# Kernel optimization log

Hardware: AMD Instinct MI355X
Metric: run time of the kernel (lower is better)

The kernel has to match this reference:

```python
import jax, jax.numpy as jnp
import numpy as np

K = 5  # kernel_size
PAD = K // 2


def _median_filter(x):
    # x: [B,1,H,W]; reflect pad then 5x5 window median (lower median of 25 elems == true median)
    B, C, H, W = x.shape
    xp = jnp.pad(x, ((0, 0), (0, 0), (PAD, PAD), (PAD, PAD)), mode='reflect')
    windows = jnp.stack([xp[:, :, dy:dy + H, dx:dx + W]
                         for dy in range(K) for dx in range(K)], axis=0)
    return jnp.median(windows, axis=0)


def _gaussian_kernel(sigma):
    c = K // 2
    coords = jnp.arange(K, dtype=jnp.float32) - c
    d2 = coords[:, None] ** 2 + coords[None, :] ** 2  # [K,K]
    kern = jnp.exp(-d2 / (2.0 * sigma ** 2)) / (2.0 * jnp.pi * sigma ** 2)
    kern = kern / kern.sum()
    return kern[None, None]  # [1,1,K,K] (OIHW, single channel, groups=1)


def setup_inputs() -> dict:
    key = jax.random.key(0)
    img = jax.random.normal(key, (8, 1024, 1024), dtype=jnp.float32)
    sigma = jnp.float32(4.0)  # learnable parameter of the Gaussian filter
    return {"img": img, "sigma": sigma}


def reference(img, sigma):
    x = img[:, None]           # [B,1,H,W]
    x = _median_filter(x)      # [B,1,H,W]
    kern = _gaussian_kernel(sigma)
    x = jax.lax.conv_general_dilated(
        x, kern, window_strides=(1, 1),
        padding=[(PAD, PAD), (PAD, PAD)],
        dimension_numbers=('NCHW', 'OIHW', 'NCHW'))
    return x[:, 0]             # [B,H,W]
```

## Files before the change

### kernel.cpp

```cpp
#include <hip/hip_runtime.h>

#define HH 1024
#define WW 1024
#define NIMG 8
#define TROWS 16

__device__ __forceinline__ float med3f(float a, float b, float c) {
    return __builtin_amdgcn_fmed3f(a, b, c);
}
__device__ __forceinline__ float min3f(float a, float b, float c) {
    return fminf(fminf(a, b), c);
}
__device__ __forceinline__ float max3f(float a, float b, float c) {
    return fmaxf(fmaxf(a, b), c);
}

__device__ __forceinline__ void top2(float a, float b, float c, float d, float e,
                                     float& r3, float& r4) {
    float m3 = med3f(a, b, c);
    float h3 = max3f(a, b, c);
    float s2 = med3f(m3, h3, d);
    float s3 = fmaxf(h3, d);
    r3 = med3f(s2, s3, e);
    r4 = fmaxf(s3, e);
}
__device__ __forceinline__ void bot2(float a, float b, float c, float d, float e,
                                     float& r0, float& r1) {
    float l3 = min3f(a, b, c);
    float m3 = med3f(a, b, c);
    float s0 = fminf(l3, d);
    float s1 = med3f(l3, m3, d);
    r0 = fminf(s0, e);
    r1 = med3f(s0, s1, e);
}
__device__ __forceinline__ void top3(float a, float b, float c, float d, float e,
                                     float& r2, float& r3, float& r4) {
    float l3 = min3f(a, b, c);
    float m3 = med3f(a, b, c);
    float h3 = max3f(a, b, c);
    float s1 = med3f(l3, m3, d);
    float s2 = med3f(m3, h3, d);
    float s3 = fmaxf(h3, d);
    r2 = med3f(s1, s2, e);
    r3 = med3f(s2, s3, e);
    r4 = fmaxf(s3, e);
}
__device__ __forceinline__ void bot3(float a, float b, float c, float d, float e,
                                     float& r0, float& r1, float& r2) {
    float l3 = min3f(a, b, c);
    float m3 = med3f(a, b, c);
    float h3 = max3f(a, b, c);
    float s0 = fminf(l3, d);
    float s1 = med3f(l3, m3, d);
    float s2 = med3f(m3, h3, d);
    r0 = fminf(s0, e);
    r1 = med3f(s0, s1, e);
    r2 = med3f(s1, s2, e);
}
__device__ __forceinline__ void mid3(float a, float b, float c, float d, float e,
                                     float& r1, float& r2, float& r3) {
    float l3 = min3f(a, b, c);
    float m3 = med3f(a, b, c);
    float h3 = max3f(a, b, c);
    float s0 = fminf(l3, d);
    float s1 = med3f(l3, m3, d);
    float s2 = med3f(m3, h3, d);
    float s3 = fmaxf(h3, d);
    r1 = med3f(s0, s1, e);
    r2 = med3f(s1, s2, e);
    r3 = med3f(s2, s3, e);
}

__device__ __forceinline__ void loadrow(const float* __restrict__ base, int r,
                                        int tid, int x0, float (&d)[8]) {
    const int rr = (r < 0) ? -r : (r >= HH ? 2 * HH - 2 - r : r);
    const float* rp = base + (size_t)rr * WW;
    const float4 A = *reinterpret_cast<const float4*>(rp + (tid == 0   ? x0 : x0 - 4));
    const float4 B = *reinterpret_cast<const float4*>(rp + x0);
    const float4 C = *reinterpret_cast<const float4*>(rp + (tid == 255 ? x0 : x0 + 4));
    d[0] = (tid == 0)   ? B.z : A.z;
    d[1] = (tid == 0)   ? B.y : A.w;
    d[2] = B.x; d[3] = B.y; d[4] = B.z; d[5] = B.w;
    d[6] = (tid == 255) ? B.z : C.x;
    d[7] = (tid == 255) ? B.y : C.y;
}

__device__ __forceinline__ void med4net(const float (&S0)[8], const float (&S1)[8],
                                        const float (&S2)[8], const float (&S3)[8],
                                        const float (&S4)[8], float (&med)[4]) {
    #pragma unroll
    for (int j = 0; j < 4; ++j) {
        float r03, r04, r12, r13, r14, r21, r22, r23, r30, r31, r32, r40, r41;
        top2(S0[j], S0[j+1], S0[j+2], S0[j+3], S0[j+4], r03, r04);
        top3(S1[j], S1[j+1], S1[j+2], S1[j+3], S1[j+4], r12, r13, r14);
        mid3(S2[j], S2[j+1], S2[j+2], S2[j+3], S2[j+4], r21, r22, r23);
        bot3(S3[j], S3[j+1], S3[j+2], S3[j+3], S3[j+4], r30, r31, r32);
        bot2(S4[j], S4[j+1], S4[j+2], S4[j+3], S4[j+4], r40, r41);
        float u = fminf(r40, r31), v = fmaxf(r40, r31);
        float w = fminf(v, r32),  x = fmaxf(v, r32);
        float ps0 = r30, ps1 = u, ps2 = w;
        float ps3 = fminf(x, r41), ps4 = fmaxf(x, r41);
        float q0 = fminf(r21, r03);
        float q1 = med3f(r21, r22, r03);
        float q2 = med3f(r22, r23, r03);
        float t1 = fminf(q1, r04);
        float t2 = med3f(q1, q2, r04);
        float t3 = med3f(q2, r23, r04);
        float t4 = fmaxf(r23, r04);
        float Y0 = fmaxf(ps0, q0);
        float Y1 = fmaxf(ps1, t1);
        float X2 = fminf(ps2, t2), Y2 = fmaxf(ps2, t2);
        float X3 = fminf(ps3, t3);
        float X4 = fminf(ps4, t4);
        float L  = max3f(X2, Y0, r12);
        float M  = med3f(X3, Y1, r13);
        float Hc = min3f(X4, Y2, r14);
        med[j] = med3f(L, M, Hc);
    }
}

template<int P>
__device__ __forceinline__ void pairstep(int y0, int tid, int x0, int lane, int w,
                                         const float* __restrict__ base,
                                         float (&ring)[8][8], float (&medr)[10][4],
                                         float (*seam)[4][10][4]) {
    constexpr int B  = P / 5;
    constexpr int RR = 2 * (P % 5);
    if constexpr (P <= 8) {
        loadrow(base, y0 + 2 + 2 * P, tid, x0, ring[(2 * P + 6) & 7]);
        loadrow(base, y0 + 3 + 2 * P, tid, x0, ring[(2 * P + 7) & 7]);
    }
    constexpr int s0 = (2*P) & 7,     s1 = (2*P + 1) & 7, s2 = (2*P + 2) & 7;
    constexpr int s3 = (2*P + 3) & 7, s4 = (2*P + 4) & 7, s5 = (2*P + 5) & 7;
    float T0[8], T1[8], T2[8], T3[8];
    #pragma unroll
    for (int c = 0; c < 8; ++c) {
        float b = ring[s1][c], cc = ring[s2][c], d = ring[s3][c], e = ring[s4][c];
        float l3 = min3f(b, cc, d);
        float m3 = med3f(b, cc, d);
        float h3 = max3f(b, cc, d);
        T0[c] = fminf(l3, e);
        T1[c] = med3f(l3, m3, e);
        T2[c] = med3f(m3, h3, e);
        T3[c] = fmaxf(h3, e);
    }
    const int m0 = y0 - 2 + 2 * P;
    float med0[4] = {0.f, 0.f, 0.f, 0.f};
    float med1[4] = {0.f, 0.f, 0.f, 0.f};
    if (m0 >= 0 && m0 < HH) {
        float S0[8], S1[8], S2[8], S3[8], S4[8];
        #pragma unroll
        for (int c = 0; c < 8; ++c) {
            float a = ring[s0][c];
            S0[c] = fminf(T0[c], a);
            S1[c] = med3f(T0[c], T1[c], a);
            S2[c] = med3f(T1[c], T2[c], a);
            S3[c] = med3f(T2[c], T3[c], a);
            S4[c] = fmaxf(T3[c], a);
        }
        med4net(S0, S1, S2, S3, S4, med0);
    }
    if (m0 + 1 >= 0 && m0 + 1 < HH) {
        float S0[8], S1[8], S2[8], S3[8], S4[8];
        #pragma unroll
        for (int c = 0; c < 8; ++c) {
            float f = ring[s5][c];
            S0[c] = fminf(T0[c], f);
            S1[c] = med3f(T0[c], T1[c], f);
            S2[c] = med3f(T1[c], T2[c], f);
            S3[c] = med3f(T2[c], T3[c], f);
            S4[c] = fmaxf(T3[c], f);
        }
        med4net(S0, S1, S2, S3, S4, med1);
    }
    #pragma unroll
    for (int j = 0; j < 4; ++j) { medr[RR][j] = med0[j]; medr[RR + 1][j] = med1[j]; }
    if (lane == 0 || lane == 63) {
        const int off = (lane == 0) ? 0 : 2;
        float e00 = (lane == 0) ? med0[0] : med0[2];
        float e01 = (lane == 0) ? med0[1] : med0[3];
        float e10 = (lane == 0) ? med1[0] : med1[2];
        float e11 = (lane == 0) ? med1[1] : med1[3];
        *reinterpret_cast<float2*>(&seam[B][w][RR][off])     = make_float2(e00, e01);
        *reinterpret_cast<float2*>(&seam[B][w][RR + 1][off]) = make_float2(e10, e11);
    }
}

template<int B>
__device__ __forceinline__ void gaussbatch(int y0, int x0, int lane, int w,
                                           float* __restrict__ obase,
                                           const float (&wv)[5],
                                           const float (&medr)[10][4],
                                           float (&hr)[6][4],
                                           const float (*seam)[4][10][4]) {
    #pragma unroll
    for (int r = 0; r < 10; ++r) {
        const int m = y0 - 2 + 10 * B + r;
        const float m0 = medr[r][0], m1 = medr[r][1];
        const float m2 = medr[r][2], m3 = medr[r][3];
        float ml0 = __shfl_up(m2, 1);
        float ml1 = __shfl_up(m3, 1);
        float mr0 = __shfl_down(m0, 1);
        float mr1 = __shfl_down(m1, 1);
        if (lane == 0) {
            if (w > 0) {
                float2 t = *reinterpret_cast<const float2*>(&seam[B][w - 1][r][2]);
                ml0 = t.x; ml1 = t.y;
            } else { ml0 = 0.f; ml1 = 0.f; }
        }
        if (lane == 63) {
            if (w < 3) {
                float2 t = *reinterpret_cast<const float2*>(&seam[B][w + 1][r][0]);
                mr0 = t.x; mr1 = t.y;
            } else { mr0 = 0.f; mr1 = 0.f; }
        }
        const float hh[8] = { ml0, ml1, m0, m1, m2, m3, mr0, mr1 };
        #pragma unroll
        for (int j = 0; j < 4; ++j) {
            float h = 0.f;
            #pragma unroll
            for (int c = 0; c < 5; ++c) h = fmaf(wv[c], hh[j + c], h);
            hr[(10 * B + r) % 6][j] = h;
        }
        if (10 * B + r >= 4) {
            const int o = m - 2;
            float a0 = 0.f, a1 = 0.f, a2 = 0.f, a3 = 0.f;
            #pragma unroll
            for (int k = 0; k < 5; ++k) {
                const int   sl = (10 * B + r - 4 + k) % 6;
                const float wy = wv[k];
                a0 = fmaf(wy, hr[sl][0], a0);
                a1 = fmaf(wy, hr[sl][1], a1);
                a2 = fmaf(wy, hr[sl][2], a2);
                a3 = fmaf(wy, hr[sl][3], a3);
            }
            *reinterpret_cast<float4*>(obase + (size_t)o * WW + x0) =
                make_float4(a0, a1, a2, a3);
        }
    }
}

__global__ __launch_bounds__(256, 2) void fused_kernel(const float* __restrict__ in,
                                                       const float* __restrict__ sig,
                                                       float* __restrict__ out) {
    const int bi   = blockIdx.x;
    const int img  = bi & 7;
    const int tile = bi >> 3;
    const int y0   = tile * TROWS;
    const int tid  = threadIdx.x;
    const int x0   = tid * 4;
    const int lane = tid & 63;
    const int w    = tid >> 6;
    const float* base  = in  + (size_t)img * HH * WW;
    float*       obase = out + (size_t)img * HH * WW;

    const float sigma  = sig[0];
    const float inv2s2 = 1.0f / (2.0f * sigma * sigma);
    const float g1 = expf(-1.0f * inv2s2);
    const float g4 = expf(-4.0f * inv2s2);
    const float sn = 1.0f + 2.0f * g1 + 2.0f * g4;
    const float wv[5] = { g4 / sn, g1 / sn, 1.0f / sn, g1 / sn, g4 / sn };

    __shared__ float seam[2][4][10][4];

    float ring[8][8];
    float medr[10][4];
    float hr[6][4];

    #pragma unroll
    for (int k = 0; k < 6; ++k) loadrow(base, y0 - 4 + k, tid, x0, ring[k]);

    pairstep<0>(y0, tid, x0, lane, w, base, ring, medr, seam);
    pairstep<1>(y0, tid, x0, lane, w, base, ring, medr, seam);
    pairstep<2>(y0, tid, x0, lane, w, base, ring, medr, seam);
    pairstep<3>(y0, tid, x0, lane, w, base, ring, medr, seam);
    pairstep<4>(y0, tid, x0, lane, w, base, ring, medr, seam);
    __syncthreads();
    gaussbatch<0>(y0, x0, lane, w, obase, wv, medr, hr, seam);
    pairstep<5>(y0, tid, x0, lane, w, base, ring, medr, seam);
    pairstep<6>(y0, tid, x0, lane, w, base, ring, medr, seam);
    pairstep<7>(y0, tid, x0, lane, w, base, ring, medr, seam);
    pairstep<8>(y0, tid, x0, lane, w, base, ring, medr, seam);
    pairstep<9>(y0, tid, x0, lane, w, base, ring, medr, seam);
    __syncthreads();
    gaussbatch<1>(y0, x0, lane, w, obase, wv, medr, hr, seam);
}

extern "C" void kernel_launch(void* const* d_in, const int* in_sizes, int n_in,
                              void* d_out, int out_size, void* d_ws, size_t ws_size,
                              hipStream_t stream) {
    const float* img = (const float*)d_in[0];
    const float* sig = (const float*)d_in[1];
    float* out = (float*)d_out;

    dim3 grid(NIMG * (HH / TROWS));
    dim3 block(256);
    hipLaunchKernelGGL(fused_kernel, grid, block, 0, stream, img, sig, out);
}
```

Before: 38.65 us.

## Halve per-thread column width and double block size to 512 threads

Each thread now produces 2 output columns instead of 4, so a block uses 512 threads (8 waves) to cover the 1024-wide row, and launch bounds request 4 blocks per CU. Per-thread register arrays (ring, medr, hr) shrink, which is meant to raise occupancy and hide load latency. In exchange, overlapping halo loads and shared column-sort work grow relative to useful output, loads become float2 instead of float4, and the shared-memory seam exchange widens to 8 waves.

Measured after the change: 46.27 us. +19.7%, slower.

```diff
diff --git a/kernel.cpp b/kernel.cpp
--- a/kernel.cpp
+++ b/kernel.cpp
@@ -4,6 +4,7 @@
 #define WW 1024
 #define NIMG 8
 #define TROWS 16
+#define NT 512
 
 __device__ __forceinline__ float med3f(float a, float b, float c) {
     return __builtin_amdgcn_fmed3f(a, b, c);
@@ -72,24 +73,24 @@
 }
 
 __device__ __forceinline__ void loadrow(const float* __restrict__ base, int r,
-                                        int tid, int x0, float (&d)[8]) {
+                                        int tid, int x0, float (&d)[6]) {
     const int rr = (r < 0) ? -r : (r >= HH ? 2 * HH - 2 - r : r);
     const float* rp = base + (size_t)rr * WW;
-    const float4 A = *reinterpret_cast<const float4*>(rp + (tid == 0   ? x0 : x0 - 4));
-    const float4 B = *reinterpret_cast<const float4*>(rp + x0);
-    const float4 C = *reinterpret_cast<const float4*>(rp + (tid == 255 ? x0 : x0 + 4));
-    d[0] = (tid == 0)   ? B.z : A.z;
-    d[1] = (tid == 0)   ? B.y : A.w;
-    d[2] = B.x; d[3] = B.y; d[4] = B.z; d[5] = B.w;
-    d[6] = (tid == 255) ? B.z : C.x;
-    d[7] = (tid == 255) ? B.y : C.y;
-}
-
-__device__ __forceinline__ void med4net(const float (&S0)[8], const float (&S1)[8],
-                                        const float (&S2)[8], const float (&S3)[8],
-                                        const float (&S4)[8], float (&med)[4]) {
-    #pragma unroll
-    for (int j = 0; j < 4; ++j) {
+    const float2 A = *reinterpret_cast<const float2*>(rp + (tid == 0      ? x0 : x0 - 2));
+    const float2 B = *reinterpret_cast<const float2*>(rp + x0);
+    const float2 C = *reinterpret_cast<const float2*>(rp + (tid == NT - 1 ? x0 : x0 + 2));
+    d[0] = (tid == 0)      ? C.x : A.x;
+    d[1] = (tid == 0)      ? B.y : A.y;
+    d[2] = B.x; d[3] = B.y;
+    d[4] = (tid == NT - 1) ? B.x : C.x;
+    d[5] = (tid == NT - 1) ? A.y : C.y;
+}
+
+__device__ __forceinline__ void med2net(const float (&S0)[6], const float (&S1)[6],
+                                        const float (&S2)[6], const float (&S3)[6],
+                                        const float (&S4)[6], float (&med)[2]) {
+    #pragma unroll
+    for (int j = 0; j < 2; ++j) {
         float r03, r04, r12, r13, r14, r21, r22, r23, r30, r31, r32, r40, r41;
         top2(S0[j], S0[j+1], S0[j+2], S0[j+3], S0[j+4], r03, r04);
         top3(S1[j], S1[j+1], S1[j+2], S1[j+3], S1[j+4], r12, r13, r14);
@@ -122,8 +123,8 @@
 template<int P>
 __device__ __forceinline__ void pairstep(int y0, int tid, int x0, int lane, int w,
                                          const float* __restrict__ base,
-                                         float (&ring)[8][8], float (&medr)[10][4],
-                                         float (*seam)[4][10][4]) {
+                                         float (&ring)[8][6], float (&medr)[10][2],
+                                         float (*seam)[8][10][4]) {
     constexpr int B  = P / 5;
     constexpr int RR = 2 * (P % 5);
     if constexpr (P <= 8) {
@@ -132,9 +133,9 @@
     }
     constexpr int s0 = (2*P) & 7,     s1 = (2*P + 1) & 7, s2 = (2*P + 2) & 7;
     constexpr int s3 = (2*P + 3) & 7, s4 = (2*P + 4) & 7, s5 = (2*P + 5) & 7;
-    float T0[8], T1[8], T2[8], T3[8];
-    #pragma unroll
-    for (int c = 0; c < 8; ++c) {
+    float T0[6], T1[6], T2[6], T3[6];
+    #pragma unroll
+    for (int c = 0; c < 6; ++c) {
         float b = ring[s1][c], cc = ring[s2][c], d = ring[s3][c], e = ring[s4][c];
         float l3 = min3f(b, cc, d);
         float m3 = med3f(b, cc, d);
@@ -145,12 +146,12 @@
         T3[c] = fmaxf(h3, e);
     }
     const int m0 = y0 - 2 + 2 * P;
-    float med0[4] = {0.f, 0.f, 0.f, 0.f};
-    float med1[4] = {0.f, 0.f, 0.f, 0.f};
+    float med0[2] = {0.f, 0.f};
+    float med1[2] = {0.f, 0.f};
     if (m0 >= 0 && m0 < HH) {
-        float S0[8], S1[8], S2[8], S3[8], S4[8];
+        float S0[6], S1[6], S2[6], S3[6], S4[6];
         #pragma unroll
-        for (int c = 0; c < 8; ++c) {
+        for (int c = 0; c < 6; ++c) {
             float a = ring[s0][c];
             S0[c] = fminf(T0[c], a);
             S1[c] = med3f(T0[c], T1[c], a);
@@ -158,12 +159,12 @@
             S3[c] = med3f(T2[c], T3[c], a);
             S4[c] = fmaxf(T3[c], a);
         }
-        med4net(S0, S1, S2, S3, S4, med0);
+        med2net(S0, S1, S2, S3, S4, med0);
     }
     if (m0 + 1 >= 0 && m0 + 1 < HH) {
-        float S0[8], S1[8], S2[8], S3[8], S4[8];
+        float S0[6], S1[6], S2[6], S3[6], S4[6];
         #pragma unroll
-        for (int c = 0; c < 8; ++c) {
+        for (int c = 0; c < 6; ++c) {
             float f = ring[s5][c];
             S0[c] = fminf(T0[c], f);
             S1[c] = med3f(T0[c], T1[c], f);
@@ -171,18 +172,14 @@
             S3[c] = med3f(T2[c], T3[c], f);
             S4[c] = fmaxf(T3[c], f);
         }
-        med4net(S0, S1, S2, S3, S4, med1);
-    }
-    #pragma unroll
-    for (int j = 0; j < 4; ++j) { medr[RR][j] = med0[j]; medr[RR + 1][j] = med1[j]; }
+        med2net(S0, S1, S2, S3, S4, med1);
+    }
+    medr[RR][0] = med0[0]; medr[RR][1] = med0[1];
+    medr[RR + 1][0] = med1[0]; medr[RR + 1][1] = med1[1];
     if (lane == 0 || lane == 63) {
         const int off = (lane == 0) ? 0 : 2;
-        float e00 = (lane == 0) ? med0[0] : med0[2];
-        float e01 = (lane == 0) ? med0[1] : med0[3];
-        float e10 = (lane == 0) ? med1[0] : med1[2];
-        float e11 = (lane == 0) ? med1[1] : med1[3];
-        *reinterpret_cast<float2*>(&seam[B][w][RR][off])     = make_float2(e00, e01);
-        *reinterpret_cast<float2*>(&seam[B][w][RR + 1][off]) = make_float2(e10, e11);
+        *reinterpret_cast<float2*>(&seam[B][w][RR][off])     = make_float2(med0[0], med0[1]);
+        *reinterpret_cast<float2*>(&seam[B][w][RR + 1][off]) = make_float2(med1[0], med1[1]);
     }
 }
 
@@ -190,16 +187,15 @@
 __device__ __forceinline__ void gaussbatch(int y0, int x0, int lane, int w,
                                            float* __restrict__ obase,
                                            const float (&wv)[5],
-                                           const float (&medr)[10][4],
-                                           float (&hr)[6][4],
-                                           const float (*seam)[4][10][4]) {
+                                           const float (&medr)[10][2],
+                                           float (&hr)[6][2],
+                                           const float (*seam)[8][10][4]) {
     #pragma unroll
     for (int r = 0; r < 10; ++r) {
         const int m = y0 - 2 + 10 * B + r;
         const float m0 = medr[r][0], m1 = medr[r][1];
-        const float m2 = medr[r][2], m3 = medr[r][3];
-        float ml0 = __shfl_up(m2, 1);
-        float ml1 = __shfl_up(m3, 1);
+        float ml0 = __shfl_up(m0, 1);
+        float ml1 = __shfl_up(m1, 1);
         float mr0 = __shfl_down(m0, 1);
         float mr1 = __shfl_down(m1, 1);
         if (lane == 0) {
@@ -209,14 +205,14 @@
             } else { ml0 = 0.f; ml1 = 0.f; }
         }
         if (lane == 63) {
-            if (w < 3) {
+            if (w < 7) {
                 float2 t = *reinterpret_cast<const float2*>(&seam[B][w + 1][r][0]);
                 mr0 = t.x; mr1 = t.y;
             } else { mr0 = 0.f; mr1 = 0.f; }
         }
-        const float hh[8] = { ml0, ml1, m0, m1, m2, m3, mr0, mr1 };
+        const float hh[6] = { ml0, ml1, m0, m1, mr0, mr1 };
         #pragma unroll
-        for (int j = 0; j < 4; ++j) {
+        for (int j = 0; j < 2; ++j) {
             float h = 0.f;
             #pragma unroll
             for (int c = 0; c < 5; ++c) h = fmaf(wv[c], hh[j + c], h);
@@ -224,31 +220,29 @@
         }
         if (10 * B + r >= 4) {
             const int o = m - 2;
-            float a0 = 0.f, a1 = 0.f, a2 = 0.f, a3 = 0.f;
+            float a0 = 0.f, a1 = 0.f;
             #pragma unroll
             for (int k = 0; k < 5; ++k) {
                 const int   sl = (10 * B + r - 4 + k) % 6;
                 const float wy = wv[k];
                 a0 = fmaf(wy, hr[sl][0], a0);
                 a1 = fmaf(wy, hr[sl][1], a1);
-                a2 = fmaf(wy, hr[sl][2], a2);
-                a3 = fmaf(wy, hr[sl][3], a3);
             }
-            *reinterpret_cast<float4*>(obase + (size_t)o * WW + x0) =
-                make_float4(a0, a1, a2, a3);
-        }
-    }
-}
-
-__global__ __launch_bounds__(256, 2) void fused_kernel(const float* __restrict__ in,
-                                                       const float* __restrict__ sig,
-                                                       float* __restrict__ out) {
+            *reinterpret_cast<float2*>(obase + (size_t)o * WW + x0) =
+                make_float2(a0, a1);
+        }
+    }
+}
+
+__global__ __launch_bounds__(NT, 4) void fused_kernel(const float* __restrict__ in,
+                                                      const float* __restrict__ sig,
+                                                      float* __restrict__ out) {
     const int bi   = blockIdx.x;
     const int img  = bi & 7;
     const int tile = bi >> 3;
     const int y0   = tile * TROWS;
     const int tid  = threadIdx.x;
-    const int x0   = tid * 4;
+    const int x0   = tid * 2;
     const int lane = tid & 63;
     const int w    = tid >> 6;
     const float* base  = in  + (size_t)img * HH * WW;
@@ -261,11 +255,11 @@
     const float sn = 1.0f + 2.0f * g1 + 2.0f * g4;
     const float wv[5] = { g4 / sn, g1 / sn, 1.0f / sn, g1 / sn, g4 / sn };
 
-    __shared__ float seam[2][4][10][4];
-
-    float ring[8][8];
-    float medr[10][4];
-    float hr[6][4];
+    __shared__ float seam[2][8][10][4];
+
+    float ring[8][6];
+    float medr[10][2];
+    float hr[6][2];
 
     #pragma unroll
     for (int k = 0; k < 6; ++k) loadrow(base, y0 - 4 + k, tid, x0, ring[k]);
@@ -294,6 +288,6 @@
     float* out = (float*)d_out;
 
     dim3 grid(NIMG * (HH / TROWS));
-    dim3 block(256);
+    dim3 block(NT);
     hipLaunchKernelGGL(fused_kernel, grid, block, 0, stream, img, sig, out);
 }
```
